# Kernel optimization log

Hardware: AMD Instinct MI355X
Metric: run time of the kernel (lower is better)

Reference implementation:

```python
import jax, jax.numpy as jnp
import numpy as np

B, L, D, NH = 32, 512, 1024, 1024
T, C = 8, 15          # tables, columns per table
E = T * (1 + C)       # 128 entities (table entity + its column entities)
NCOL = T * C          # 120 column slots == max_entities
K = L // E            # 4 tokens per entity span
TOPK = 6


def setup_inputs() -> dict:
    key = jax.random.key(0)
    ks = jax.random.split(key, 12)
    std = 0.02
    q_enc = jax.random.normal(ks[0], (B, L, D), jnp.float32)
    # contiguous variable-length-style spans: entity e covers tokens [e*K, (e+1)*K)
    entity_tok_idx = jnp.arange(E * K, dtype=jnp.int32).reshape(E, K)
    # entity layout per batch: [tbl0, col0..col14, tbl1, col15..., ...]
    ent = np.arange(E).reshape(T, 1 + C)
    col_entity_idx = jnp.asarray(ent[:, 1:].reshape(-1), jnp.int32)   # [NCOL]
    col_table_idx = jnp.asarray(np.repeat(ent[:, 0], C), jnp.int32)   # [NCOL]
    return {
        "q_enc": q_enc,
        "entity_tok_idx": entity_tok_idx,
        "col_entity_idx": col_entity_idx,
        "col_table_idx": col_table_idx,
        "W_table": jax.random.normal(ks[1], (D, D), jnp.float32) * std,
        "b_table": jnp.zeros((D,), jnp.float32),
        "W_col": jax.random.normal(ks[2], (D, D), jnp.float32) * std,
        "b_col": jnp.zeros((D,), jnp.float32),
        "W_o1": jax.random.normal(ks[3], (D, NH), jnp.float32) * std,
        "b_o1": jnp.zeros((NH,), jnp.float32),
        "W_o2": jax.random.normal(ks[4], (NH, 1), jnp.float32) * std,
        "b_o2": jnp.zeros((1,), jnp.float32),
        "W_t1": jax.random.normal(ks[5], (D, NH), jnp.float32) * std,
        "b_t1": jnp.zeros((NH,), jnp.float32),
        "W_t2": jax.random.normal(ks[6], (NH, TOPK), jnp.float32) * std,
        "b_t2": jnp.zeros((TOPK,), jnp.float32),
    }


def reference(q_enc, entity_tok_idx, col_entity_idx, col_table_idx,
              W_table, b_table, W_col, b_col,
              W_o1, b_o1, W_o2, b_o2,
              W_t1, b_t1, W_t2, b_t2):
    # ragged per-entity token gather + sum pooling (pad+sum in original)
    # q_enc: [B, L, D]; gather -> [B, E, K, D]; segment reduce over K
    encoded_entity = jnp.take(q_enc, entity_tok_idx, axis=1).sum(axis=2)  # [B, E, D]
    # per-column fusion: col_linear(col entity) + table_linear(parent table entity)
    tbl = jnp.einsum("bed,df->bef", encoded_entity[:, col_table_idx], W_table) + b_table
    col = jnp.einsum("bed,df->bef", encoded_entity[:, col_entity_idx], W_col) + b_col
    fused = col + tbl                                                    # [B, NCOL, D]
    att = (jax.nn.relu(fused @ W_o1 + b_o1) @ W_o2 + b_o2)[..., 0]       # [B, NCOL]
    cls = q_enc[:, 0, :]                                                 # [B, D]
    topk = jax.nn.sigmoid(jax.nn.relu(cls @ W_t1 + b_t1) @ W_t2 + b_t2)  # [B, 6]
    return att, topk
```

## Files before the change

### kernel.cpp

```cpp
#include <hip/hip_runtime.h>
#include <hip/hip_bf16.h>

#define BB 32
#define LL 512
#define DD 1024
#define NHD 1024
#define EE 128
#define NCOL 120
#define KTOK 4
#define TOPKN 6
#define MROWS (BB * NCOL)

typedef __attribute__((ext_vector_type(8))) _Float16 f16x8;
typedef __attribute__((ext_vector_type(4))) float f32x4;

__device__ inline ushort f2h(float x) {
    _Float16 h = (_Float16)x;
    union { _Float16 h; ushort u; } c;
    c.h = h;
    return c.u;
}

__global__ __launch_bounds__(256) void ee_kernel(const float* __restrict__ q,
                                                 const int* __restrict__ tok,
                                                 ushort* __restrict__ ee,
                                                 float* __restrict__ att,
                                                 const float* __restrict__ b_o2,
                                                 float* __restrict__ H,
                                                 const float* __restrict__ b_t1) {
    int be = blockIdx.x;
    int b  = be >> 7;
    int e  = be & 127;
    int t  = threadIdx.x;

    if (be < 15) {
        att[be * 256 + t] = b_o2[0];
    } else if (be < 15 + 128) {
        int j = (be - 15) * 256 + t;
        H[j] = b_t1[j & (NHD - 1)];
    }

    const float* qb = q + (size_t)b * LL * DD;
    int t0 = tok[e * KTOK + 0];
    int t1 = tok[e * KTOK + 1];
    int t2 = tok[e * KTOK + 2];
    int t3 = tok[e * KTOK + 3];
    int f = t * 4;
    float4 a = *(const float4*)(qb + (size_t)t0 * DD + f);
    float4 bv = *(const float4*)(qb + (size_t)t1 * DD + f);
    float4 c = *(const float4*)(qb + (size_t)t2 * DD + f);
    float4 d = *(const float4*)(qb + (size_t)t3 * DD + f);
    ushort4 o;
    o.x = f2h(a.x + bv.x + c.x + d.x);
    o.y = f2h(a.y + bv.y + c.y + d.y);
    o.z = f2h(a.z + bv.z + c.z + d.z);
    o.w = f2h(a.w + bv.w + c.w + d.w);
    *(ushort4*)(ee + (size_t)be * DD + f) = o;
}

__global__ __launch_bounds__(256) void pack_w_kernel(
    const float* __restrict__ W0, const float* __restrict__ W1f,
    const float* __restrict__ W2f, ushort* __restrict__ pk0,
    ushort* __restrict__ pk1, ushort* __restrict__ pk2) {
    const float* W = blockIdx.y == 0 ? W0 : (blockIdx.y == 1 ? W1f : W2f);
    ushort* pk     = blockIdx.y == 0 ? pk0 : (blockIdx.y == 1 ? pk1 : pk2);
    int idx = blockIdx.x * 256 + threadIdx.x;
    int l  = idx & 63;
    int kb = (idx >> 6) & 31;
    int nb = idx >> 11;
    int row = kb * 32 + (l >> 4) * 8;
    int col = nb * 16 + (l & 15);
    ushort o[8];
#pragma unroll
    for (int j = 0; j < 8; ++j)
        o[j] = f2h(W[(size_t)(row + j) * NHD + col]);
    ulong2 v;
    v.x = ((ulong)o[0]) | ((ulong)o[1] << 16) | ((ulong)o[2] << 32) | ((ulong)o[3] << 48);
    v.y = ((ulong)o[4]) | ((ulong)o[5] << 16) | ((ulong)o[6] << 32) | ((ulong)o[7] << 48);
    *(ulong2*)(pk + (size_t)idx * 8) = v;
}

#define DEF_MFMA(A0, A1, B0, B1)                                                \
    {                                                                           \
        acc00 = __builtin_amdgcn_mfma_f32_16x16x32_f16(A0, B0, acc00, 0, 0, 0); \
        acc01 = __builtin_amdgcn_mfma_f32_16x16x32_f16(A0, B1, acc01, 0, 0, 0); \
        acc10 = __builtin_amdgcn_mfma_f32_16x16x32_f16(A1, B0, acc10, 0, 0, 0); \
        acc11 = __builtin_amdgcn_mfma_f32_16x16x32_f16(A1, B1, acc11, 0, 0, 0); \
    }

#define GEMM_PIPE(ar0, ar1, W)                                                  \
    {                                                                           \
        const ushort* a0p = (ar0);                                              \
        const ushort* a1p = (ar1);                                              \
        const ushort* wp  = (W);                                                \
        _LD(Aa0, Aa1, Ba0, Ba1, 0)                                              \
        _LD(Ab0, Ab1, Bb0, Bb1, 1)                                              \
        _LD(Ac0, Ac1, Bc0, Bc1, 2)                                              \
        _Pragma("unroll 1")                                                     \
        for (int kb = 0; kb < 27; kb += 3) {                                    \
            DEF_MFMA(Aa0, Aa1, Ba0, Ba1) _LD(Aa0, Aa1, Ba0, Ba1, kb + 3)        \
            DEF_MFMA(Ab0, Ab1, Bb0, Bb1) _LD(Ab0, Ab1, Bb0, Bb1, kb + 4)        \
            DEF_MFMA(Ac0, Ac1, Bc0, Bc1) _LD(Ac0, Ac1, Bc0, Bc1, kb + 5)        \
        }                                                                       \
        DEF_MFMA(Aa0, Aa1, Ba0, Ba1) _LD(Aa0, Aa1, Ba0, Ba1, 30)                \
        DEF_MFMA(Ab0, Ab1, Bb0, Bb1) _LD(Ab0, Ab1, Bb0, Bb1, 31)                \
        DEF_MFMA(Ac0, Ac1, Bc0, Bc1)                                            \
        DEF_MFMA(Aa0, Aa1, Ba0, Ba1)                                            \
        DEF_MFMA(Ab0, Ab1, Bb0, Bb1)                                            \
    }

#define _LD(A0, A1, B0, B1, kb)                                                 \
    {                                                                           \
        A0 = *(const f16x8*)(a0p + (kb) * 32 + koff);                           \
        A1 = *(const f16x8*)(a1p + (kb) * 32 + koff);                           \
        B0 = *(const f16x8*)(wp + (((size_t)nb0 * 32 + (kb)) * 64 + l) * 8);    \
        B1 = *(const f16x8*)(wp + (((size_t)(nb0 + 1) * 32 + (kb)) * 64 + l) * 8); \
    }

__global__ __launch_bounds__(256) void gemm1_kernel(
    const ushort* __restrict__ ee, const int* __restrict__ ci, const int* __restrict__ ti,
    const ushort* __restrict__ Wc_pk, const ushort* __restrict__ Wt_pk,
    const float* __restrict__ bc, const float* __restrict__ bt,
    ushort* __restrict__ fused) {
    int t = threadIdx.x;
    int l = t & 63;
    int w = t >> 6;
    int wm = w >> 1, wn = w & 1;
    int row0 = blockIdx.x * 64 + wm * 32;
    int col0 = blockIdx.y * 64 + wn * 32;
    int nb0  = col0 >> 4;
    int koff = (l >> 4) * 8;

    const ushort* arow0[2];
    const ushort* arow1[2];
#pragma unroll
    for (int m = 0; m < 2; ++m) {
        int r = row0 + m * 16 + (l & 15);
        int b = r / NCOL;
        int i = r - b * NCOL;
        arow0[m] = ee + ((size_t)(b * EE + ci[i])) * DD;
        arow1[m] = ee + ((size_t)(b * EE + ti[i])) * DD;
    }

    f32x4 acc00 = {}, acc01 = {}, acc10 = {}, acc11 = {};
    f16x8 Aa0, Aa1, Ba0, Ba1, Ab0, Ab1, Bb0, Bb1, Ac0, Ac1, Bc0, Bc1;

    GEMM_PIPE(arow0[0], arow0[1], Wc_pk)
    GEMM_PIPE(arow1[0], arow1[1], Wt_pk)

    float badd[2];
#pragma unroll
    for (int n = 0; n < 2; ++n) {
        int c = col0 + n * 16 + (l & 15);
        badd[n] = bc[c] + bt[c];
    }
    int rlane = (l >> 4) * 4;
    f32x4 accm[2][2] = {{acc00, acc01}, {acc10, acc11}};
#pragma unroll
    for (int m = 0; m < 2; ++m)
#pragma unroll
        for (int n = 0; n < 2; ++n) {
            int c = col0 + n * 16 + (l & 15);
#pragma unroll
            for (int j = 0; j < 4; ++j) {
                int r = row0 + m * 16 + rlane + j;
                fused[(size_t)r * NHD + c] = f2h(accm[m][n][j] + badd[n]);
            }
        }
}

__global__ __launch_bounds__(256) void gemm2_kernel(
    const ushort* __restrict__ fused, const ushort* __restrict__ W1_pk,
    const float* __restrict__ b1, const float* __restrict__ W2,
    float* __restrict__ att) {
    int t = threadIdx.x;
    int l = t & 63;
    int w = t >> 6;
    int wm = w >> 1, wn = w & 1;
    int row0 = blockIdx.x * 64 + wm * 32;
    int col0 = blockIdx.y * 64 + wn * 32;
    int nb0  = col0 >> 4;
    int koff = (l >> 4) * 8;

    const ushort* arow[2];
#pragma unroll
    for (int m = 0; m < 2; ++m)
        arow[m] = fused + (size_t)(row0 + m * 16 + (l & 15)) * NHD;

    f32x4 acc00 = {}, acc01 = {}, acc10 = {}, acc11 = {};
    f16x8 Aa0, Aa1, Ba0, Ba1, Ab0, Ab1, Bb0, Bb1, Ac0, Ac1, Bc0, Bc1;

    GEMM_PIPE(arow[0], arow[1], W1_pk)

    float bo[2], wo[2];
#pragma unroll
    for (int n = 0; n < 2; ++n) {
        int c = col0 + n * 16 + (l & 15);
        bo[n] = b1[c];
        wo[n] = W2[c];
    }
    int rlane = (l >> 4) * 4;
    f32x4 accm[2][2] = {{acc00, acc01}, {acc10, acc11}};
#pragma unroll
    for (int m = 0; m < 2; ++m) {
#pragma unroll
        for (int j = 0; j < 4; ++j) {
            float p = 0.f;
#pragma unroll
            for (int n = 0; n < 2; ++n) {
                float h = fmaxf(accm[m][n][j] + bo[n], 0.f);
                p = fmaf(h, wo[n], p);
            }
            p += __shfl_xor(p, 1);
            p += __shfl_xor(p, 2);
            p += __shfl_xor(p, 4);
            p += __shfl_xor(p, 8);
            if ((l & 15) == 0)
                atomicAdd(&att[row0 + m * 16 + rlane + j], p);
        }
    }
}

__global__ __launch_bounds__(256) void topk_h_kernel(const float* __restrict__ q,
                                                     const float* __restrict__ W1,
                                                     float* __restrict__ H) {
    __shared__ float cls[BB][128];
    __shared__ float wsh[128][17];
    int f0 = blockIdx.x * 16;
    int k0 = blockIdx.y * 128;
    int t = threadIdx.x;
#pragma unroll
    for (int m = 0; m < 16; ++m) {
        int idx = t + m * 256;
        int b = idx >> 7, d = idx & 127;
        cls[b][d] = q[(size_t)b * LL * DD + k0 + d];
    }
#pragma unroll
    for (int m = 0; m < 8; ++m) {
        int idx = t + m * 256;
        int r = idx >> 4, c = idx & 15;
        wsh[r][c] = W1[(size_t)(k0 + r) * NHD + f0 + c];
    }
    __syncthreads();
    int f = t & 15;
    int b0 = t >> 4;
#pragma unroll
    for (int h = 0; h < 2; ++h) {
        int b = b0 + h * 16;
        float s = 0.f;
#pragma unroll 8
        for (int d = 0; d < 128; ++d)
            s = fmaf(cls[b][d], wsh[d][f], s);
        atomicAdd(&H[(size_t)b * NHD + f0 + f], s);
    }
}

__global__ __launch_bounds__(256) void topk_out_kernel(
    const float* __restrict__ H, const float* __restrict__ W2,
    const float* __restrict__ b2, float* __restrict__ outp) {
    __shared__ float red[4][TOPKN];
    int b = blockIdx.x;
    int t = threadIdx.x;
    float part[TOPKN] = {};
#pragma unroll
    for (int m = 0; m < 4; ++m) {
        int f = t + m * 256;
        float h = fmaxf(H[(size_t)b * NHD + f], 0.f);
#pragma unroll
        for (int k = 0; k < TOPKN; ++k)
            part[k] = fmaf(h, W2[f * TOPKN + k], part[k]);
    }
#pragma unroll
    for (int k = 0; k < TOPKN; ++k) {
        float v = part[k];
        for (int off = 1; off < 64; off <<= 1) v += __shfl_xor(v, off);
        part[k] = v;
    }
    int wave = t >> 6, lane = t & 63;
    if (lane == 0)
#pragma unroll
        for (int k = 0; k < TOPKN; ++k) red[wave][k] = part[k];
    __syncthreads();
    if (t == 0)
#pragma unroll
        for (int k = 0; k < TOPKN; ++k) {
            float s = red[0][k] + red[1][k] + red[2][k] + red[3][k] + b2[k];
            outp[b * TOPKN + k] = 1.f / (1.f + __expf(-s));
        }
}

extern "C" void kernel_launch(void* const* d_in, const int* in_sizes, int n_in,
                              void* d_out, int out_size, void* d_ws, size_t ws_size,
                              hipStream_t stream) {
    const float* q_enc   = (const float*)d_in[0];
    const int*   etok    = (const int*)  d_in[1];
    const int*   ci      = (const int*)  d_in[2];
    const int*   ti      = (const int*)  d_in[3];
    const float* W_table = (const float*)d_in[4];
    const float* b_table = (const float*)d_in[5];
    const float* W_col   = (const float*)d_in[6];
    const float* b_col   = (const float*)d_in[7];
    const float* W_o1    = (const float*)d_in[8];
    const float* b_o1    = (const float*)d_in[9];
    const float* W_o2    = (const float*)d_in[10];
    const float* b_o2    = (const float*)d_in[11];
    const float* W_t1    = (const float*)d_in[12];
    const float* b_t1    = (const float*)d_in[13];
    const float* W_t2    = (const float*)d_in[14];
    const float* b_t2    = (const float*)d_in[15];

    float* outp = (float*)d_out;
    float* att  = outp;
    float* topk = outp + MROWS;

    char* ws = (char*)d_ws;
    ushort* ee_h    = (ushort*)(ws);
    ushort* fused   = (ushort*)(ws + 8388608);
    ushort* Wc_pk   = (ushort*)(ws + 16252928);
    ushort* Wt_pk   = (ushort*)(ws + 18350080);
    ushort* Wo1_pk  = (ushort*)(ws + 20447232);
    float*  H       = (float*) (ws + 22544384);

    hipLaunchKernelGGL(ee_kernel, dim3(BB * EE), dim3(256), 0, stream,
                       q_enc, etok, ee_h, att, b_o2, H, b_t1);
    hipLaunchKernelGGL(pack_w_kernel, dim3(512, 3), dim3(256), 0, stream,
                       W_col, W_table, W_o1, Wc_pk, Wt_pk, Wo1_pk);
    hipLaunchKernelGGL(gemm1_kernel, dim3(MROWS / 64, NHD / 64), dim3(256), 0, stream,
                       ee_h, ci, ti, Wc_pk, Wt_pk, b_col, b_table, fused);
    hipLaunchKernelGGL(gemm2_kernel, dim3(MROWS / 64, NHD / 64), dim3(256), 0, stream,
                       fused, Wo1_pk, b_o1, W_o2, att);
    hipLaunchKernelGGL(topk_h_kernel, dim3(64, 8), dim3(256), 0, stream, q_enc, W_t1, H);
    hipLaunchKernelGGL(topk_out_kernel, dim3(BB), dim3(256), 0, stream, H, W_t2, b_t2, topk);
}
```

Before: 233.2 us.

## Stage GEMM tiles in LDS with 128x128 blocks and register prefetch

```diff
diff --git a/kernel.cpp b/kernel.cpp
--- a/kernel.cpp
+++ b/kernel.cpp
@@ -10,6 +10,8 @@
 #define KTOK 4
 #define TOPKN 6
 #define MROWS (BB * NCOL)
+#define NKB1 64
+#define NKB2 32
 
 typedef __attribute__((ext_vector_type(8))) _Float16 f16x8;
 typedef __attribute__((ext_vector_type(4))) float f32x4;
@@ -80,135 +82,161 @@
     *(ulong2*)(pk + (size_t)idx * 8) = v;
 }
 
-#define DEF_MFMA(A0, A1, B0, B1)                                                \
-    {                                                                           \
-        acc00 = __builtin_amdgcn_mfma_f32_16x16x32_f16(A0, B0, acc00, 0, 0, 0); \
-        acc01 = __builtin_amdgcn_mfma_f32_16x16x32_f16(A0, B1, acc01, 0, 0, 0); \
-        acc10 = __builtin_amdgcn_mfma_f32_16x16x32_f16(A1, B0, acc10, 0, 0, 0); \
-        acc11 = __builtin_amdgcn_mfma_f32_16x16x32_f16(A1, B1, acc11, 0, 0, 0); \
-    }
-
-#define GEMM_PIPE(ar0, ar1, W)                                                  \
-    {                                                                           \
-        const ushort* a0p = (ar0);                                              \
-        const ushort* a1p = (ar1);                                              \
-        const ushort* wp  = (W);                                                \
-        _LD(Aa0, Aa1, Ba0, Ba1, 0)                                              \
-        _LD(Ab0, Ab1, Bb0, Bb1, 1)                                              \
-        _LD(Ac0, Ac1, Bc0, Bc1, 2)                                              \
-        _Pragma("unroll 1")                                                     \
-        for (int kb = 0; kb < 27; kb += 3) {                                    \
-            DEF_MFMA(Aa0, Aa1, Ba0, Ba1) _LD(Aa0, Aa1, Ba0, Ba1, kb + 3)        \
-            DEF_MFMA(Ab0, Ab1, Bb0, Bb1) _LD(Ab0, Ab1, Bb0, Bb1, kb + 4)        \
-            DEF_MFMA(Ac0, Ac1, Bc0, Bc1) _LD(Ac0, Ac1, Bc0, Bc1, kb + 5)        \
-        }                                                                       \
-        DEF_MFMA(Aa0, Aa1, Ba0, Ba1) _LD(Aa0, Aa1, Ba0, Ba1, 30)                \
-        DEF_MFMA(Ab0, Ab1, Bb0, Bb1) _LD(Ab0, Ab1, Bb0, Bb1, 31)                \
-        DEF_MFMA(Ac0, Ac1, Bc0, Bc1)                                            \
-        DEF_MFMA(Aa0, Aa1, Ba0, Ba1)                                            \
-        DEF_MFMA(Ab0, Ab1, Bb0, Bb1)                                            \
-    }
-
-#define _LD(A0, A1, B0, B1, kb)                                                 \
-    {                                                                           \
-        A0 = *(const f16x8*)(a0p + (kb) * 32 + koff);                           \
-        A1 = *(const f16x8*)(a1p + (kb) * 32 + koff);                           \
-        B0 = *(const f16x8*)(wp + (((size_t)nb0 * 32 + (kb)) * 64 + l) * 8);    \
-        B1 = *(const f16x8*)(wp + (((size_t)(nb0 + 1) * 32 + (kb)) * 64 + l) * 8); \
-    }
-
 __global__ __launch_bounds__(256) void gemm1_kernel(
     const ushort* __restrict__ ee, const int* __restrict__ ci, const int* __restrict__ ti,
     const ushort* __restrict__ Wc_pk, const ushort* __restrict__ Wt_pk,
     const float* __restrict__ bc, const float* __restrict__ bt,
     ushort* __restrict__ fused) {
+    __shared__ ushort As[128 * 40];
+    __shared__ ushort Bs[8 * 512];
+
     int t = threadIdx.x;
     int l = t & 63;
     int w = t >> 6;
     int wm = w >> 1, wn = w & 1;
-    int row0 = blockIdx.x * 64 + wm * 32;
-    int col0 = blockIdx.y * 64 + wn * 32;
+    int bx = blockIdx.x >> 3;
+    int by = blockIdx.x & 7;
+    int row0 = bx * 128, col0 = by * 128;
     int nb0  = col0 >> 4;
-    int koff = (l >> 4) * 8;
-
-    const ushort* arow0[2];
-    const ushort* arow1[2];
-#pragma unroll
-    for (int m = 0; m < 2; ++m) {
-        int r = row0 + m * 16 + (l & 15);
-        int b = r / NCOL;
-        int i = r - b * NCOL;
-        arow0[m] = ee + ((size_t)(b * EE + ci[i])) * DD;
-        arow1[m] = ee + ((size_t)(b * EE + ti[i])) * DD;
-    }
-
-    f32x4 acc00 = {}, acc01 = {}, acc10 = {}, acc11 = {};
-    f16x8 Aa0, Aa1, Ba0, Ba1, Ab0, Ab1, Bb0, Bb1, Ac0, Ac1, Bc0, Bc1;
-
-    GEMM_PIPE(arow0[0], arow0[1], Wc_pk)
-    GEMM_PIPE(arow1[0], arow1[1], Wt_pk)
-
-    float badd[2];
-#pragma unroll
-    for (int n = 0; n < 2; ++n) {
-        int c = col0 + n * 16 + (l & 15);
-        badd[n] = bc[c] + bt[c];
-    }
-    int rlane = (l >> 4) * 4;
-    f32x4 accm[2][2] = {{acc00, acc01}, {acc10, acc11}};
-#pragma unroll
-    for (int m = 0; m < 2; ++m)
-#pragma unroll
-        for (int n = 0; n < 2; ++n) {
-            int c = col0 + n * 16 + (l & 15);
-#pragma unroll
-            for (int j = 0; j < 4; ++j) {
-                int r = row0 + m * 16 + rlane + j;
-                fused[(size_t)r * NHD + c] = f2h(accm[m][n][j] + badd[n]);
-            }
+
+    int sr = t >> 1;
+    int ss = t & 1;
+    int Rg = row0 + sr;
+    int bq = Rg / NCOL, iq = Rg - bq * NCOL;
+    const ushort* ap0 = ee + ((size_t)(bq * EE + ci[iq])) * DD;
+    const ushort* ap1 = ee + ((size_t)(bq * EE + ti[iq])) * DD;
+
+    f32x4 acc[4][4] = {};
+    f16x8 av0, av1, bv0, bv1;
+
+#define G1_LOAD(kb)                                                              \
+    {                                                                            \
+        int kk = (kb) & 31;                                                      \
+        const ushort* ap = ((kb) >> 5) ? ap1 : ap0;                              \
+        const ushort* Wp = ((kb) >> 5) ? Wt_pk : Wc_pk;                          \
+        av0 = *(const f16x8*)(ap + kk * 32 + ss * 8);                            \
+        av1 = *(const f16x8*)(ap + kk * 32 + (ss + 2) * 8);                      \
+        bv0 = *(const f16x8*)(Wp + ((size_t)(nb0 + w) * 32 + kk) * 512 + l * 8); \
+        bv1 = *(const f16x8*)(Wp + ((size_t)(nb0 + 4 + w) * 32 + kk) * 512 + l * 8); \
+    }
+
+    G1_LOAD(0)
+#pragma unroll 1
+    for (int kb = 0; kb < NKB1; ++kb) {
+        __syncthreads();
+        *(f16x8*)&As[sr * 40 + ss * 8]       = av0;
+        *(f16x8*)&As[sr * 40 + (ss + 2) * 8] = av1;
+        *(f16x8*)&Bs[w * 512 + l * 8]        = bv0;
+        *(f16x8*)&Bs[(4 + w) * 512 + l * 8]  = bv1;
+        __syncthreads();
+        int kbn = (kb + 1 < NKB1) ? kb + 1 : kb;
+        G1_LOAD(kbn)
+        f16x8 af[4], bf[4];
+#pragma unroll
+        for (int m = 0; m < 4; ++m)
+            af[m] = *(const f16x8*)&As[(wm * 64 + m * 16 + (l & 15)) * 40 + (l >> 4) * 8];
+#pragma unroll
+        for (int n = 0; n < 4; ++n)
+            bf[n] = *(const f16x8*)&Bs[(wn * 4 + n) * 512 + l * 8];
+#pragma unroll
+        for (int m = 0; m < 4; ++m)
+#pragma unroll
+            for (int n = 0; n < 4; ++n)
+                acc[m][n] = __builtin_amdgcn_mfma_f32_16x16x32_f16(
+                    af[m], bf[n], acc[m][n], 0, 0, 0);
+    }
+#undef G1_LOAD
+
+    int lr = (l >> 4) * 4;
+#pragma unroll
+    for (int n = 0; n < 4; ++n) {
+        int c = col0 + wn * 64 + n * 16 + (l & 15);
+        float badd = bc[c] + bt[c];
+#pragma unroll
+        for (int m = 0; m < 4; ++m) {
+            int rbase = row0 + wm * 64 + m * 16 + lr;
+#pragma unroll
+            for (int j = 0; j < 4; ++j)
+                fused[(size_t)(rbase + j) * NHD + c] = f2h(acc[m][n][j] + badd);
         }
+    }
 }
 
 __global__ __launch_bounds__(256) void gemm2_kernel(
     const ushort* __restrict__ fused, const ushort* __restrict__ W1_pk,
     const float* __restrict__ b1, const float* __restrict__ W2,
     float* __restrict__ att) {
+    __shared__ ushort As[128 * 40];
+    __shared__ ushort Bs[8 * 512];
+
     int t = threadIdx.x;
     int l = t & 63;
     int w = t >> 6;
     int wm = w >> 1, wn = w & 1;
-    int row0 = blockIdx.x * 64 + wm * 32;
-    int col0 = blockIdx.y * 64 + wn * 32;
+    int bx = blockIdx.x >> 3;
+    int by = blockIdx.x & 7;
+    int row0 = bx * 128, col0 = by * 128;
     int nb0  = col0 >> 4;
-    int koff = (l >> 4) * 8;
-
-    const ushort* arow[2];
-#pragma unroll
-    for (int m = 0; m < 2; ++m)
-        arow[m] = fused + (size_t)(row0 + m * 16 + (l & 15)) * NHD;
-
-    f32x4 acc00 = {}, acc01 = {}, acc10 = {}, acc11 = {};
-    f16x8 Aa0, Aa1, Ba0, Ba1, Ab0, Ab1, Bb0, Bb1, Ac0, Ac1, Bc0, Bc1;
-
-    GEMM_PIPE(arow[0], arow[1], W1_pk)
-
-    float bo[2], wo[2];
-#pragma unroll
-    for (int n = 0; n < 2; ++n) {
-        int c = col0 + n * 16 + (l & 15);
+
+    int sr = t >> 1;
+    int ss = t & 1;
+    const ushort* ap = fused + (size_t)(row0 + sr) * NHD;
+
+    f32x4 acc[4][4] = {};
+    f16x8 av0, av1, bv0, bv1;
+
+#define G2_LOAD(kb)                                                              \
+    {                                                                            \
+        int kk = (kb);                                                           \
+        av0 = *(const f16x8*)(ap + kk * 32 + ss * 8);                            \
+        av1 = *(const f16x8*)(ap + kk * 32 + (ss + 2) * 8);                      \
+        bv0 = *(const f16x8*)(W1_pk + ((size_t)(nb0 + w) * 32 + kk) * 512 + l * 8); \
+        bv1 = *(const f16x8*)(W1_pk + ((size_t)(nb0 + 4 + w) * 32 + kk) * 512 + l * 8); \
+    }
+
+    G2_LOAD(0)
+#pragma unroll 1
+    for (int kb = 0; kb < NKB2; ++kb) {
+        __syncthreads();
+        *(f16x8*)&As[sr * 40 + ss * 8]       = av0;
+        *(f16x8*)&As[sr * 40 + (ss + 2) * 8] = av1;
+        *(f16x8*)&Bs[w * 512 + l * 8]        = bv0;
+        *(f16x8*)&Bs[(4 + w) * 512 + l * 8]  = bv1;
+        __syncthreads();
+        int kbn = (kb + 1 < NKB2) ? kb + 1 : kb;
+        G2_LOAD(kbn)
+        f16x8 af[4], bf[4];
+#pragma unroll
+        for (int m = 0; m < 4; ++m)
+            af[m] = *(const f16x8*)&As[(wm * 64 + m * 16 + (l & 15)) * 40 + (l >> 4) * 8];
+#pragma unroll
+        for (int n = 0; n < 4; ++n)
+            bf[n] = *(const f16x8*)&Bs[(wn * 4 + n) * 512 + l * 8];
+#pragma unroll
+        for (int m = 0; m < 4; ++m)
+#pragma unroll
+            for (int n = 0; n < 4; ++n)
+                acc[m][n] = __builtin_amdgcn_mfma_f32_16x16x32_f16(
+                    af[m], bf[n], acc[m][n], 0, 0, 0);
+    }
+#undef G2_LOAD
+
+    float bo[4], wo[4];
+#pragma unroll
+    for (int n = 0; n < 4; ++n) {
+        int c = col0 + wn * 64 + n * 16 + (l & 15);
         bo[n] = b1[c];
         wo[n] = W2[c];
     }
-    int rlane = (l >> 4) * 4;
-    f32x4 accm[2][2] = {{acc00, acc01}, {acc10, acc11}};
-#pragma unroll
-    for (int m = 0; m < 2; ++m) {
+    int lr = (l >> 4) * 4;
+#pragma unroll
+    for (int m = 0; m < 4; ++m) {
 #pragma unroll
         for (int j = 0; j < 4; ++j) {
             float p = 0.f;
 #pragma unroll
-            for (int n = 0; n < 2; ++n) {
-                float h = fmaxf(accm[m][n][j] + bo[n], 0.f);
+            for (int n = 0; n < 4; ++n) {
+                float h = fmaxf(acc[m][n][j] + bo[n], 0.f);
                 p = fmaf(h, wo[n], p);
             }
             p += __shfl_xor(p, 1);
@@ -216,7 +244,7 @@
             p += __shfl_xor(p, 4);
             p += __shfl_xor(p, 8);
             if ((l & 15) == 0)
-                atomicAdd(&att[row0 + m * 16 + rlane + j], p);
+                atomicAdd(&att[row0 + wm * 64 + m * 16 + lr + j], p);
         }
     }
 }
@@ -325,9 +353,9 @@
                        q_enc, etok, ee_h, att, b_o2, H, b_t1);
     hipLaunchKernelGGL(pack_w_kernel, dim3(512, 3), dim3(256), 0, stream,
                        W_col, W_table, W_o1, Wc_pk, Wt_pk, Wo1_pk);
-    hipLaunchKernelGGL(gemm1_kernel, dim3(MROWS / 64, NHD / 64), dim3(256), 0, stream,
+    hipLaunchKernelGGL(gemm1_kernel, dim3((MROWS / 128) * (NHD / 128)), dim3(256), 0, stream,
                        ee_h, ci, ti, Wc_pk, Wt_pk, b_col, b_table, fused);
-    hipLaunchKernelGGL(gemm2_kernel, dim3(MROWS / 64, NHD / 64), dim3(256), 0, stream,
+    hipLaunchKernelGGL(gemm2_kernel, dim3((MROWS / 128) * (NHD / 128)), dim3(256), 0, stream,
                        fused, Wo1_pk, b_o1, W_o2, att);
     hipLaunchKernelGGL(topk_h_kernel, dim3(64, 8), dim3(256), 0, stream, q_enc, W_t1, H);
     hipLaunchKernelGGL(topk_out_kernel, dim3(BB), dim3(256), 0, stream, H, W_t2, b_t2, topk);
```

Result: faster. 215.8 us (-7.4%).

## Stage A tiles through double-buffered LDS and linearize GEMM grid

Applied to the files above, without the earlier changes.

```diff
diff --git a/kernel.cpp b/kernel.cpp
--- a/kernel.cpp
+++ b/kernel.cpp
@@ -10,6 +10,8 @@
 #define KTOK 4
 #define TOPKN 6
 #define MROWS (BB * NCOL)
+#define NKB1 64
+#define NKB2 32
 
 typedef __attribute__((ext_vector_type(8))) _Float16 f16x8;
 typedef __attribute__((ext_vector_type(4))) float f32x4;
@@ -80,126 +82,173 @@
     *(ulong2*)(pk + (size_t)idx * 8) = v;
 }
 
-#define DEF_MFMA(A0, A1, B0, B1)                                                \
-    {                                                                           \
-        acc00 = __builtin_amdgcn_mfma_f32_16x16x32_f16(A0, B0, acc00, 0, 0, 0); \
-        acc01 = __builtin_amdgcn_mfma_f32_16x16x32_f16(A0, B1, acc01, 0, 0, 0); \
-        acc10 = __builtin_amdgcn_mfma_f32_16x16x32_f16(A1, B0, acc10, 0, 0, 0); \
-        acc11 = __builtin_amdgcn_mfma_f32_16x16x32_f16(A1, B1, acc11, 0, 0, 0); \
-    }
-
-#define GEMM_PIPE(ar0, ar1, W)                                                  \
-    {                                                                           \
-        const ushort* a0p = (ar0);                                              \
-        const ushort* a1p = (ar1);                                              \
-        const ushort* wp  = (W);                                                \
-        _LD(Aa0, Aa1, Ba0, Ba1, 0)                                              \
-        _LD(Ab0, Ab1, Bb0, Bb1, 1)                                              \
-        _LD(Ac0, Ac1, Bc0, Bc1, 2)                                              \
-        _Pragma("unroll 1")                                                     \
-        for (int kb = 0; kb < 27; kb += 3) {                                    \
-            DEF_MFMA(Aa0, Aa1, Ba0, Ba1) _LD(Aa0, Aa1, Ba0, Ba1, kb + 3)        \
-            DEF_MFMA(Ab0, Ab1, Bb0, Bb1) _LD(Ab0, Ab1, Bb0, Bb1, kb + 4)        \
-            DEF_MFMA(Ac0, Ac1, Bc0, Bc1) _LD(Ac0, Ac1, Bc0, Bc1, kb + 5)        \
-        }                                                                       \
-        DEF_MFMA(Aa0, Aa1, Ba0, Ba1) _LD(Aa0, Aa1, Ba0, Ba1, 30)                \
-        DEF_MFMA(Ab0, Ab1, Bb0, Bb1) _LD(Ab0, Ab1, Bb0, Bb1, 31)                \
-        DEF_MFMA(Ac0, Ac1, Bc0, Bc1)                                            \
-        DEF_MFMA(Aa0, Aa1, Ba0, Ba1)                                            \
-        DEF_MFMA(Ab0, Ab1, Bb0, Bb1)                                            \
-    }
-
-#define _LD(A0, A1, B0, B1, kb)                                                 \
-    {                                                                           \
-        A0 = *(const f16x8*)(a0p + (kb) * 32 + koff);                           \
-        A1 = *(const f16x8*)(a1p + (kb) * 32 + koff);                           \
-        B0 = *(const f16x8*)(wp + (((size_t)nb0 * 32 + (kb)) * 64 + l) * 8);    \
-        B1 = *(const f16x8*)(wp + (((size_t)(nb0 + 1) * 32 + (kb)) * 64 + l) * 8); \
-    }
-
 __global__ __launch_bounds__(256) void gemm1_kernel(
     const ushort* __restrict__ ee, const int* __restrict__ ci, const int* __restrict__ ti,
     const ushort* __restrict__ Wc_pk, const ushort* __restrict__ Wt_pk,
     const float* __restrict__ bc, const float* __restrict__ bt,
     ushort* __restrict__ fused) {
+    __shared__ ushort As0[64 * 40];
+    __shared__ ushort As1[64 * 40];
+
     int t = threadIdx.x;
     int l = t & 63;
     int w = t >> 6;
     int wm = w >> 1, wn = w & 1;
-    int row0 = blockIdx.x * 64 + wm * 32;
-    int col0 = blockIdx.y * 64 + wn * 32;
-    int nb0  = col0 >> 4;
+    int bx = blockIdx.x >> 4;
+    int by = blockIdx.x & 15;
+    int row0 = bx * 64, col0 = by * 64;
+    int nbw  = (col0 >> 4) + wn * 2;
     int koff = (l >> 4) * 8;
 
-    const ushort* arow0[2];
-    const ushort* arow1[2];
-#pragma unroll
-    for (int m = 0; m < 2; ++m) {
-        int r = row0 + m * 16 + (l & 15);
-        int b = r / NCOL;
-        int i = r - b * NCOL;
-        arow0[m] = ee + ((size_t)(b * EE + ci[i])) * DD;
-        arow1[m] = ee + ((size_t)(b * EE + ti[i])) * DD;
-    }
+    int arow = t >> 2;
+    int seg  = t & 3;
+    int Rg = row0 + arow;
+    int bq = Rg / NCOL, iq = Rg - bq * NCOL;
+    const ushort* ap0 = ee + ((size_t)(bq * EE + ci[iq])) * DD;
+    const ushort* ap1 = ee + ((size_t)(bq * EE + ti[iq])) * DD;
 
     f32x4 acc00 = {}, acc01 = {}, acc10 = {}, acc11 = {};
-    f16x8 Aa0, Aa1, Ba0, Ba1, Ab0, Ab1, Bb0, Bb1, Ac0, Ac1, Bc0, Bc1;
-
-    GEMM_PIPE(arow0[0], arow0[1], Wc_pk)
-    GEMM_PIPE(arow1[0], arow1[1], Wt_pk)
-
-    float badd[2];
+    f16x8 sA, ba0, ba1, bb0, bb1;
+
+#define LOADA(S, kb)                                                             \
+    {                                                                            \
+        int kk = (kb) & 31;                                                      \
+        const ushort* ap = ((kb) >> 5) ? ap1 : ap0;                              \
+        S = *(const f16x8*)(ap + kk * 32 + seg * 8);                             \
+    }
+#define LOADB(B0, B1, kb)                                                        \
+    {                                                                            \
+        int kk = (kb) & 31;                                                      \
+        const ushort* Wp = ((kb) >> 5) ? Wt_pk : Wc_pk;                          \
+        B0 = *(const f16x8*)(Wp + ((size_t)nbw * 32 + kk) * 512 + l * 8);        \
+        B1 = *(const f16x8*)(Wp + ((size_t)(nbw + 1) * 32 + kk) * 512 + l * 8);  \
+    }
+#define WRITEA(BUF, S) { *(f16x8*)&BUF[arow * 40 + seg * 8] = S; }
+#define COMP(BUF, B0, B1)                                                        \
+    {                                                                            \
+        f16x8 a0 = *(const f16x8*)&BUF[(wm * 32 + (l & 15)) * 40 + koff];        \
+        f16x8 a1 = *(const f16x8*)&BUF[(wm * 32 + 16 + (l & 15)) * 40 + koff];   \
+        acc00 = __builtin_amdgcn_mfma_f32_16x16x32_f16(a0, B0, acc00, 0, 0, 0);  \
+        acc01 = __builtin_amdgcn_mfma_f32_16x16x32_f16(a0, B1, acc01, 0, 0, 0);  \
+        acc10 = __builtin_amdgcn_mfma_f32_16x16x32_f16(a1, B0, acc10, 0, 0, 0);  \
+        acc11 = __builtin_amdgcn_mfma_f32_16x16x32_f16(a1, B1, acc11, 0, 0, 0);  \
+    }
+
+    LOADA(sA, 0)
+    WRITEA(As0, sA)
+    LOADA(sA, 1)
+    LOADB(ba0, ba1, 0)
+    LOADB(bb0, bb1, 1)
+    __syncthreads();
+
+#pragma unroll 1
+    for (int kb = 0; kb < NKB1; kb += 2) {
+        WRITEA(As1, sA)
+        { int kn = kb + 2 < NKB1 ? kb + 2 : NKB1 - 1; LOADA(sA, kn) }
+        COMP(As0, ba0, ba1)
+        { int kn = kb + 2 < NKB1 ? kb + 2 : NKB1 - 1; LOADB(ba0, ba1, kn) }
+        __syncthreads();
+        WRITEA(As0, sA)
+        { int kn = kb + 3 < NKB1 ? kb + 3 : NKB1 - 1; LOADA(sA, kn) }
+        COMP(As1, bb0, bb1)
+        { int kn = kb + 3 < NKB1 ? kb + 3 : NKB1 - 1; LOADB(bb0, bb1, kn) }
+        __syncthreads();
+    }
+#undef LOADA
+#undef LOADB
+#undef WRITEA
+#undef COMP
+
+    int lr = (l >> 4) * 4;
+    f32x4 accm[2][2] = {{acc00, acc01}, {acc10, acc11}};
 #pragma unroll
     for (int n = 0; n < 2; ++n) {
-        int c = col0 + n * 16 + (l & 15);
-        badd[n] = bc[c] + bt[c];
-    }
-    int rlane = (l >> 4) * 4;
-    f32x4 accm[2][2] = {{acc00, acc01}, {acc10, acc11}};
-#pragma unroll
-    for (int m = 0; m < 2; ++m)
-#pragma unroll
-        for (int n = 0; n < 2; ++n) {
-            int c = col0 + n * 16 + (l & 15);
-#pragma unroll
-            for (int j = 0; j < 4; ++j) {
-                int r = row0 + m * 16 + rlane + j;
-                fused[(size_t)r * NHD + c] = f2h(accm[m][n][j] + badd[n]);
-            }
+        int c = col0 + wn * 32 + n * 16 + (l & 15);
+        float badd = bc[c] + bt[c];
+#pragma unroll
+        for (int m = 0; m < 2; ++m) {
+            int rbase = row0 + wm * 32 + m * 16 + lr;
+#pragma unroll
+            for (int j = 0; j < 4; ++j)
+                fused[(size_t)(rbase + j) * NHD + c] = f2h(accm[m][n][j] + badd);
         }
+    }
 }
 
 __global__ __launch_bounds__(256) void gemm2_kernel(
     const ushort* __restrict__ fused, const ushort* __restrict__ W1_pk,
     const float* __restrict__ b1, const float* __restrict__ W2,
     float* __restrict__ att) {
+    __shared__ ushort As0[64 * 40];
+    __shared__ ushort As1[64 * 40];
+
     int t = threadIdx.x;
     int l = t & 63;
     int w = t >> 6;
     int wm = w >> 1, wn = w & 1;
-    int row0 = blockIdx.x * 64 + wm * 32;
-    int col0 = blockIdx.y * 64 + wn * 32;
-    int nb0  = col0 >> 4;
+    int bx = blockIdx.x >> 4;
+    int by = blockIdx.x & 15;
+    int row0 = bx * 64, col0 = by * 64;
+    int nbw  = (col0 >> 4) + wn * 2;
     int koff = (l >> 4) * 8;
 
-    const ushort* arow[2];
-#pragma unroll
-    for (int m = 0; m < 2; ++m)
-        arow[m] = fused + (size_t)(row0 + m * 16 + (l & 15)) * NHD;
+    int arow = t >> 2;
+    int seg  = t & 3;
+    const ushort* ap = fused + (size_t)(row0 + arow) * NHD;
 
     f32x4 acc00 = {}, acc01 = {}, acc10 = {}, acc11 = {};
-    f16x8 Aa0, Aa1, Ba0, Ba1, Ab0, Ab1, Bb0, Bb1, Ac0, Ac1, Bc0, Bc1;
-
-    GEMM_PIPE(arow[0], arow[1], W1_pk)
+    f16x8 sA, ba0, ba1, bb0, bb1;
+
+#define LOADA(S, kb)  { S = *(const f16x8*)(ap + (kb) * 32 + seg * 8); }
+#define LOADB(B0, B1, kb)                                                        \
+    {                                                                            \
+        B0 = *(const f16x8*)(W1_pk + ((size_t)nbw * 32 + (kb)) * 512 + l * 8);   \
+        B1 = *(const f16x8*)(W1_pk + ((size_t)(nbw + 1) * 32 + (kb)) * 512 + l * 8); \
+    }
+#define WRITEA(BUF, S) { *(f16x8*)&BUF[arow * 40 + seg * 8] = S; }
+#define COMP(BUF, B0, B1)                                                        \
+    {                                                                            \
+        f16x8 a0 = *(const f16x8*)&BUF[(wm * 32 + (l & 15)) * 40 + koff];        \
+        f16x8 a1 = *(const f16x8*)&BUF[(wm * 32 + 16 + (l & 15)) * 40 + koff];   \
+        acc00 = __builtin_amdgcn_mfma_f32_16x16x32_f16(a0, B0, acc00, 0, 0, 0);  \
+        acc01 = __builtin_amdgcn_mfma_f32_16x16x32_f16(a0, B1, acc01, 0, 0, 0);  \
+        acc10 = __builtin_amdgcn_mfma_f32_16x16x32_f16(a1, B0, acc10, 0, 0, 0);  \
+        acc11 = __builtin_amdgcn_mfma_f32_16x16x32_f16(a1, B1, acc11, 0, 0, 0);  \
+    }
+
+    LOADA(sA, 0)
+    WRITEA(As0, sA)
+    LOADA(sA, 1)
+    LOADB(ba0, ba1, 0)
+    LOADB(bb0, bb1, 1)
+    __syncthreads();
+
+#pragma unroll 1
+    for (int kb = 0; kb < NKB2; kb += 2) {
+        WRITEA(As1, sA)
+        { int kn = kb + 2 < NKB2 ? kb + 2 : NKB2 - 1; LOADA(sA, kn) }
+        COMP(As0, ba0, ba1)
+        { int kn = kb + 2 < NKB2 ? kb + 2 : NKB2 - 1; LOADB(ba0, ba1, kn) }
+        __syncthreads();
+        WRITEA(As0, sA)
+        { int kn = kb + 3 < NKB2 ? kb + 3 : NKB2 - 1; LOADA(sA, kn) }
+        COMP(As1, bb0, bb1)
+        { int kn = kb + 3 < NKB2 ? kb + 3 : NKB2 - 1; LOADB(bb0, bb1, kn) }
+        __syncthreads();
+    }
+#undef LOADA
+#undef LOADB
+#undef WRITEA
+#undef COMP
 
     float bo[2], wo[2];
 #pragma unroll
     for (int n = 0; n < 2; ++n) {
-        int c = col0 + n * 16 + (l & 15);
+        int c = col0 + wn * 32 + n * 16 + (l & 15);
         bo[n] = b1[c];
         wo[n] = W2[c];
     }
-    int rlane = (l >> 4) * 4;
+    int lr = (l >> 4) * 4;
     f32x4 accm[2][2] = {{acc00, acc01}, {acc10, acc11}};
 #pragma unroll
     for (int m = 0; m < 2; ++m) {
@@ -216,7 +265,7 @@
             p += __shfl_xor(p, 4);
             p += __shfl_xor(p, 8);
             if ((l & 15) == 0)
-                atomicAdd(&att[row0 + m * 16 + rlane + j], p);
+                atomicAdd(&att[row0 + wm * 32 + m * 16 + lr + j], p);
         }
     }
 }
@@ -325,9 +374,9 @@
                        q_enc, etok, ee_h, att, b_o2, H, b_t1);
     hipLaunchKernelGGL(pack_w_kernel, dim3(512, 3), dim3(256), 0, stream,
                        W_col, W_table, W_o1, Wc_pk, Wt_pk, Wo1_pk);
-    hipLaunchKernelGGL(gemm1_kernel, dim3(MROWS / 64, NHD / 64), dim3(256), 0, stream,
+    hipLaunchKernelGGL(gemm1_kernel, dim3((MROWS / 64) * (NHD / 64)), dim3(256), 0, stream,
                        ee_h, ci, ti, Wc_pk, Wt_pk, b_col, b_table, fused);
-    hipLaunchKernelGGL(gemm2_kernel, dim3(MROWS / 64, NHD / 64), dim3(256), 0, stream,
+    hipLaunchKernelGGL(gemm2_kernel, dim3((MROWS / 64) * (NHD / 64)), dim3(256), 0, stream,
                        fused, Wo1_pk, b_o1, W_o2, att);
     hipLaunchKernelGGL(topk_h_kernel, dim3(64, 8), dim3(256), 0, stream, q_enc, W_t1, H);
     hipLaunchKernelGGL(topk_out_kernel, dim3(BB), dim3(256), 0, stream, H, W_t2, b_t2, topk);
```

Result: faster. 197.3 us (-15.4%).
